# Kernel optimization log

Measured on AMD Instinct MI355X. Metric: run time of the kernel, lower is better.

The kernel has to match this reference:

```python
import jax, jax.numpy as jnp
import numpy as np

D, P, S, E = 200, 200, 150, 150  # drugs, proteins, diseases, side-effects
EMB = 256

def setup_inputs() -> dict:
    key = jax.random.key(0)
    ks = jax.random.split(key, 10)
    s = 0.05
    type_mask = jnp.concatenate([
        jnp.zeros(D, jnp.int64) if False else jnp.full((D,), 0, jnp.int32),
        jnp.full((P,), 1, jnp.int32),
        jnp.full((S,), 2, jnp.int32),
        jnp.full((E,), 3, jnp.int32)]).astype(jnp.int32)
    return {
        'type_mask': type_mask,
        'entity_embedding': jax.random.normal(ks[0], (D + P + S + E, EMB)) * s,
        'relation_embedding': jax.random.normal(ks[1], (1200, EMB)) * s,
        'W_ent': jax.random.normal(ks[2], (EMB, EMB)) * s,
        'W_rel': jax.random.normal(ks[3], (EMB, EMB)) * s,
        'W1': jax.random.normal(ks[4], (2 * EMB, 1024)) * s,
        'b1': jnp.zeros((1024,)),
        'W2': jax.random.normal(ks[5], (1024, 512)) * s,
        'b2': jnp.zeros((512,)),
        'W3': jax.random.normal(ks[6], (512, 2)) * s,
        'b3': jnp.zeros((2,)),
    }

def _pair_softmax(a, b, W1, b1, W2, b2, W3, b3):
    # classifier(concat(a[i], b[j])) for the full cartesian product.
    # First linear is decomposed: W1 @ [a;b] = a@W1a + b@W1b (same math,
    # avoids materializing the [Na*Nb, 2*EMB] concat tensor).
    W1a, W1b = W1[:EMB], W1[EMB:]
    ha = a @ W1a                      # [Na, 1024]
    hb = b @ W1b                      # [Nb, 1024]
    h = jax.nn.relu(ha[:, None, :] + hb[None, :, :] + b1)  # [Na, Nb, 1024]
    h = jax.nn.relu(h @ W2 + b2)      # [Na, Nb, 512]
    logits = h @ W3 + b3              # [Na, Nb, 2]
    Na, Nb = a.shape[0], b.shape[0]
    return jax.nn.softmax(logits.reshape(Na * Nb, 2), axis=-1)

def reference(type_mask, entity_embedding, relation_embedding, W_ent, W_rel,
              W1, b1, W2, b2, W3, b3):
    tm = np.asarray(type_mask)  # concrete, block-structured type ids
    idx = [np.nonzero(tm == t)[0] for t in range(4)]
    # project embeddings (project_on path; nn.Linear: x @ W)
    ent = entity_embedding @ W_ent
    _rel = relation_embedding @ W_rel  # computed in original forward, unused (graph_on off)
    drug, prot, dis, se = (ent[idx[0]], ent[idx[1]], ent[idx[2]], ent[idx[3]])
    cls = lambda a, b: _pair_softmax(a, b, W1, b1, W2, b2, W3, b3)
    out_dp = cls(drug, prot)
    out_dd = cls(drug, drug)
    out_ds = cls(drug, dis)
    out_de = cls(drug, se)
    out_ps = cls(prot, dis)
    out_pp = cls(prot, prot)
    out_pd = cls(prot, drug)
    out_ed = cls(se, drug)
    out_sp = cls(dis, prot)
    out_sd = cls(dis, drug)
    return (out_dp, out_dd, out_ds, out_de, out_ps, out_pp, out_pd,
            out_ed, out_sp, out_sd, drug)
```

## Files before the change

### kernel.cpp

```cpp
#include <hip/hip_runtime.h>
#include <hip/hip_bf16.h>

typedef __attribute__((ext_vector_type(4))) float floatx4;
typedef __attribute__((ext_vector_type(8))) __bf16 bf16x8;
typedef unsigned short ushort_t;

#define NENT  700
#define EMB   256
#define KDIM  1024
#define NDIM  512
#define HROWS 720
#define NPAIR 340000

#define WS_HA   0
#define WS_HB   (WS_HA + HROWS*KDIM*2)
#define WS_W2H  (WS_HB + HROWS*KDIM*2)
#define WS_ENT  (WS_W2H + NDIM*KDIM*2)
#define WS_LG   (WS_ENT + NENT*EMB*4)

__device__ __forceinline__ float ldin(const void* p, int i, int isbf) {
    return isbf ? __bfloat162float(((const __hip_bfloat16*)p)[i])
                : ((const float*)p)[i];
}

__device__ __forceinline__ int detect_bf16(const ushort_t* __restrict__ w) {
    int t = threadIdx.x & 63;
    int e = (w[2*t] >> 7) & 0xFF;
    unsigned long long m = __ballot(e >= 100 && e <= 126);
    return (__popcll(m) >= 48) ? 1 : 0;
}

#define LDS_BARRIER() do { __builtin_amdgcn_s_waitcnt(0xC07F); __builtin_amdgcn_s_barrier(); } while (0)

__global__ void entprep_kernel(const void* __restrict__ E, const void* __restrict__ Went,
                               const void* __restrict__ W2,
                               float* __restrict__ ent, __hip_bfloat16* __restrict__ W2H,
                               void* __restrict__ out) {
    int isbf = detect_bf16((const ushort_t*)E);
    if (blockIdx.x < 88) {
        int ib = blockIdx.x * 8, t = threadIdx.x;
        __shared__ float rows[8][EMB];
#pragma unroll
        for (int r = 0; r < 8; ++r) {
            int i = ib + r;
            rows[r][t] = (i < NENT) ? ldin(E, i*EMB + t, isbf) : 0.f;
        }
        __syncthreads();
        float acc[8] = {0.f,0.f,0.f,0.f,0.f,0.f,0.f,0.f};
        if (isbf) {
            const __hip_bfloat16* W = (const __hip_bfloat16*)Went;
            for (int k = 0; k < EMB; ++k) {
                float w = __bfloat162float(W[k*EMB + t]);
#pragma unroll
                for (int r = 0; r < 8; ++r) acc[r] += rows[r][k] * w;
            }
        } else {
            const float* W = (const float*)Went;
            for (int k = 0; k < EMB; ++k) {
                float w = W[k*EMB + t];
#pragma unroll
                for (int r = 0; r < 8; ++r) acc[r] += rows[r][k] * w;
            }
        }
#pragma unroll
        for (int r = 0; r < 8; ++r) {
            int i = ib + r;
            if (i < NENT) {
                ent[i*EMB + t] = acc[r];
                if (i < 200) {
                    if (isbf) ((__hip_bfloat16*)out)[680000 + i*EMB + t] = __float2bfloat16(acc[r]);
                    else      ((float*)out)[680000 + i*EMB + t] = acc[r];
                }
            }
        }
    } else {
        int g = (blockIdx.x - 88)*256 + threadIdx.x;
        int lane = g & 63, f = (g >> 6) & 15, kc = (g >> 10) & 31, half = g >> 15;
        int l15 = lane & 15, quad = lane >> 4;
        int n = half*256 + f*16 + l15;
        bf16x8 v;
#pragma unroll
        for (int j = 0; j < 8; ++j) {
            int k = kc*32 + quad*8 + j;
            v[j] = (__bf16)ldin(W2, k*NDIM + n, isbf);
        }
        *(bf16x8*)(W2H + (size_t)g*8) = v;
    }
}

__global__ void hab_kernel(const float* __restrict__ ent, const void* __restrict__ E,
                           const void* __restrict__ W1, const void* __restrict__ b1,
                           __hip_bfloat16* __restrict__ HA, __hip_bfloat16* __restrict__ HB) {
    int isbf = detect_bf16((const ushort_t*)E);
    int part = blockIdx.y;
    int ib = blockIdx.x * 16;
    int t = threadIdx.x;
    __shared__ float rows[16][EMB];
#pragma unroll
    for (int r = 0; r < 16; ++r) {
        int i = ib + r;
        rows[r][t] = (i < NENT) ? ent[i*EMB + t] : 0.f;
    }
    __syncthreads();
    float acc[16][4];
#pragma unroll
    for (int r = 0; r < 16; ++r)
#pragma unroll
        for (int p = 0; p < 4; ++p) acc[r][p] = 0.f;

    int wbase = part*EMB*KDIM;
    if (isbf) {
        const __hip_bfloat16* W = (const __hip_bfloat16*)W1;
        for (int k = 0; k < EMB; ++k) {
            float w[4];
#pragma unroll
            for (int p = 0; p < 4; ++p) w[p] = __bfloat162float(W[wbase + k*KDIM + t + p*256]);
#pragma unroll
            for (int r = 0; r < 16; ++r) {
                float e = rows[r][k];
#pragma unroll
                for (int p = 0; p < 4; ++p) acc[r][p] += e * w[p];
            }
        }
    } else {
        const float* W = (const float*)W1;
        for (int k = 0; k < EMB; ++k) {
            float w[4];
#pragma unroll
            for (int p = 0; p < 4; ++p) w[p] = W[wbase + k*KDIM + t + p*256];
#pragma unroll
            for (int r = 0; r < 16; ++r) {
                float e = rows[r][k];
#pragma unroll
                for (int p = 0; p < 4; ++p) acc[r][p] += e * w[p];
            }
        }
    }
    __hip_bfloat16* HX = part ? HB : HA;
#pragma unroll
    for (int r = 0; r < 16; ++r) {
#pragma unroll
        for (int p = 0; p < 4; ++p) {
            int n = t + p*256;
            float v = acc[r][p];
            if (!part) v += ldin(b1, n, isbf);
            HX[(ib + r)*KDIM + n] = __float2bfloat16(v);
        }
    }
}

union U8 { bf16x8 v; unsigned u[4]; };

__device__ __forceinline__ bf16x8 mk_af3(bf16x8 ha, bf16x8 hb) {
    U8 r;
#pragma unroll
    for (int j = 0; j < 4; ++j) {
        float x0 = fmaxf((float)ha[2*j]   + (float)hb[2*j],   0.f);
        float x1 = fmaxf((float)ha[2*j+1] + (float)hb[2*j+1], 0.f);
        unsigned u0 = __float_as_uint(x0) + 0x8000u;
        unsigned u1 = __float_as_uint(x1) + 0x8000u;
#if defined(__has_builtin) && __has_builtin(__builtin_amdgcn_perm)
        r.u[j] = __builtin_amdgcn_perm(u1, u0, 0x07060302u);
#else
        r.u[j] = (u0 >> 16) | (u1 & 0xFFFF0000u);
#endif
    }
    return r.v;
}

#define MFMA(a, b, c) __builtin_amdgcn_mfma_f32_16x16x32_bf16((a), (b), (c), 0, 0, 0)

__global__ __launch_bounds__(512, 2) void pair_kernel(
        const ushort_t* __restrict__ HA, const ushort_t* __restrict__ HB,
        const ushort_t* __restrict__ W2H, const void* __restrict__ E,
        const void* __restrict__ b2, const void* __restrict__ W3,
        const void* __restrict__ b3, void* __restrict__ out) {

    const int blkEnd[10] = {650,1300,1800,2300,2800,3450,4100,4594,5088,5582};
    const int aB[10]  = {0,0,0,0,200,200,200,550,400,400};
    const int bB[10]  = {200,0,400,550,400,200,0,0,200,0};
    const int NaT[10] = {200,200,200,200,200,200,200,150,150,150};
    const int NbT[10] = {200,200,150,150,150,200,200,200,200,200};
    const int jTl[10] = {13,13,10,10,10,13,13,13,13,13};
    const int oOf[10] = {0,80000,160000,220000,280000,340000,420000,500000,560000,620000};

    __shared__ __align__(16) unsigned char sAF[16384];
    __shared__ float lgt[8][64][2];

    int bid = blockIdx.x;
    int ty = 0;
    while (bid >= blkEnd[ty]) ty++;
    int lb = bid - (ty ? blkEnd[ty-1] : 0);
    int jT = jTl[ty];
    int it = lb / jT;
    int jt = lb - it*jT;
    int i0 = aB[ty] + it*4;
    int j0 = bB[ty] + jt*16;

    int tid  = threadIdx.x;
    int lane = tid & 63;
    int w    = tid >> 6;
    int w3_  = w & 3;
    int wh   = w >> 2;
    int l15  = lane & 15;
    int quad = lane >> 4;
    int kb   = (bid*7) & 31;

    const char* WB = (const char*)W2H + ((size_t)(wh*512 + w3_*4))*1024 + lane*16;
    const ushort_t* HBp = HB + (j0 + l15)*KDIM + quad*8;
    const ushort_t* HAp = HA + (i0 + w3_)*KDIM + quad*8;

    floatx4 acc[4][4];
#pragma unroll
    for (int mf = 0; mf < 4; ++mf)
#pragma unroll
        for (int nf = 0; nf < 4; ++nf) acc[mf][nf] = (floatx4){0.f,0.f,0.f,0.f};

    int k0 = kb, k1 = (kb + 1) & 31;
    bf16x8 Bc0 = *(const bf16x8*)(WB + (size_t)k0*16384);
    bf16x8 Bc1 = *(const bf16x8*)(WB + (size_t)k0*16384 + 1024);
    bf16x8 Bc2 = *(const bf16x8*)(WB + (size_t)k0*16384 + 2048);
    bf16x8 Bc3 = *(const bf16x8*)(WB + (size_t)k0*16384 + 3072);
    bf16x8 Bn0 = *(const bf16x8*)(WB + (size_t)k1*16384);
    bf16x8 Bn1 = *(const bf16x8*)(WB + (size_t)k1*16384 + 1024);
    bf16x8 Bn2 = *(const bf16x8*)(WB + (size_t)k1*16384 + 2048);
    bf16x8 Bn3 = *(const bf16x8*)(WB + (size_t)k1*16384 + 3072);

    int kg0 = (kb + wh) & 31;
    bf16x8 ha = *(const bf16x8*)(HAp + kg0*32);
    bf16x8 hb = *(const bf16x8*)(HBp + kg0*32);

#pragma unroll 2
    for (int ph = 0; ph < 16; ++ph) {
        char* sW = (char*)sAF + (ph & 1)*8192 + w*1024 + lane*16;
        *(bf16x8*)sW = mk_af3(ha, hb);
        int kgn = (kb + 2*(ph + 1) + wh) & 31;
        ha = *(const bf16x8*)(HAp + kgn*32);
        hb = *(const bf16x8*)(HBp + kgn*32);
        LDS_BARRIER();

        const char* sR = (const char*)sAF + (ph & 1)*8192 + lane*16;
        int kn2 = (kb + 2*ph + 2) & 31;
        int kn3 = (kb + 2*ph + 3) & 31;
        {
            bf16x8 a0 = *(const bf16x8*)(sR);
            bf16x8 a1 = *(const bf16x8*)(sR + 1024);
            bf16x8 a2 = *(const bf16x8*)(sR + 2048);
            bf16x8 a3 = *(const bf16x8*)(sR + 3072);
            acc[0][0] = MFMA(a0, Bc0, acc[0][0]); acc[1][0] = MFMA(a1, Bc0, acc[1][0]);
            acc[2][0] = MFMA(a2, Bc0, acc[2][0]); acc[3][0] = MFMA(a3, Bc0, acc[3][0]);
            acc[0][1] = MFMA(a0, Bc1, acc[0][1]); acc[1][1] = MFMA(a1, Bc1, acc[1][1]);
            acc[2][1] = MFMA(a2, Bc1, acc[2][1]); acc[3][1] = MFMA(a3, Bc1, acc[3][1]);
            acc[0][2] = MFMA(a0, Bc2, acc[0][2]); acc[1][2] = MFMA(a1, Bc2, acc[1][2]);
            acc[2][2] = MFMA(a2, Bc2, acc[2][2]); acc[3][2] = MFMA(a3, Bc2, acc[3][2]);
            acc[0][3] = MFMA(a0, Bc3, acc[0][3]); acc[1][3] = MFMA(a1, Bc3, acc[1][3]);
            acc[2][3] = MFMA(a2, Bc3, acc[2][3]); acc[3][3] = MFMA(a3, Bc3, acc[3][3]);
        }
        Bc0 = *(const bf16x8*)(WB + (size_t)kn2*16384);
        Bc1 = *(const bf16x8*)(WB + (size_t)kn2*16384 + 1024);
        Bc2 = *(const bf16x8*)(WB + (size_t)kn2*16384 + 2048);
        Bc3 = *(const bf16x8*)(WB + (size_t)kn2*16384 + 3072);
        {
            bf16x8 a0 = *(const bf16x8*)(sR + 4096);
            bf16x8 a1 = *(const bf16x8*)(sR + 4096 + 1024);
            bf16x8 a2 = *(const bf16x8*)(sR + 4096 + 2048);
            bf16x8 a3 = *(const bf16x8*)(sR + 4096 + 3072);
            acc[0][0] = MFMA(a0, Bn0, acc[0][0]); acc[1][0] = MFMA(a1, Bn0, acc[1][0]);
            acc[2][0] = MFMA(a2, Bn0, acc[2][0]); acc[3][0] = MFMA(a3, Bn0, acc[3][0]);
            acc[0][1] = MFMA(a0, Bn1, acc[0][1]); acc[1][1] = MFMA(a1, Bn1, acc[1][1]);
            acc[2][1] = MFMA(a2, Bn1, acc[2][1]); acc[3][1] = MFMA(a3, Bn1, acc[3][1]);
            acc[0][2] = MFMA(a0, Bn2, acc[0][2]); acc[1][2] = MFMA(a1, Bn2, acc[1][2]);
            acc[2][2] = MFMA(a2, Bn2, acc[2][2]); acc[3][2] = MFMA(a3, Bn2, acc[3][2]);
            acc[0][3] = MFMA(a0, Bn3, acc[0][3]); acc[1][3] = MFMA(a1, Bn3, acc[1][3]);
            acc[2][3] = MFMA(a2, Bn3, acc[2][3]); acc[3][3] = MFMA(a3, Bn3, acc[3][3]);
        }
        Bn0 = *(const bf16x8*)(WB + (size_t)kn3*16384);
        Bn1 = *(const bf16x8*)(WB + (size_t)kn3*16384 + 1024);
        Bn2 = *(const bf16x8*)(WB + (size_t)kn3*16384 + 2048);
        Bn3 = *(const bf16x8*)(WB + (size_t)kn3*16384 + 3072);
    }

    int isbf = detect_bf16((const ushort_t*)E);
    int nb = wh*256 + w3_*64;
    float b2v[4], wa[4], wb[4];
#pragma unroll
    for (int nf = 0; nf < 4; ++nf) {
        int n = nb + nf*16 + l15;
        b2v[nf] = ldin(b2, n, isbf);
        wa[nf]  = ldin(W3, 2*n, isbf);
        wb[nf]  = ldin(W3, 2*n+1, isbf);
    }
#pragma unroll
    for (int mf = 0; mf < 4; ++mf) {
        float s0[4] = {0.f,0.f,0.f,0.f};
        float s1[4] = {0.f,0.f,0.f,0.f};
#pragma unroll
        for (int nf = 0; nf < 4; ++nf) {
            floatx4 c = acc[mf][nf];
#pragma unroll
            for (int r = 0; r < 4; ++r) {
                float v = fmaxf(c[r] + b2v[nf], 0.f);
                s0[r] += v * wa[nf];
                s1[r] += v * wb[nf];
            }
        }
#pragma unroll
        for (int off = 1; off < 16; off <<= 1) {
#pragma unroll
            for (int r = 0; r < 4; ++r) {
                s0[r] += __shfl_xor(s0[r], off, 64);
                s1[r] += __shfl_xor(s1[r], off, 64);
            }
        }
        if (l15 == 0) {
#pragma unroll
            for (int r = 0; r < 4; ++r) {
                int p = mf*16 + quad*4 + r;
                lgt[w][p][0] = s0[r];
                lgt[w][p][1] = s1[r];
            }
        }
    }
    __syncthreads();

    if (tid < 64) {
        int p = tid;
        float l0 = 0.f, l1 = 0.f;
#pragma unroll
        for (int ww = 0; ww < 8; ++ww) { l0 += lgt[ww][p][0]; l1 += lgt[ww][p][1]; }
        l0 += ldin(b3, 0, isbf);
        l1 += ldin(b3, 1, isbf);
        int pi = it*4 + (p >> 4), pj = jt*16 + (p & 15);
        if (pi < NaT[ty] && pj < NbT[ty]) {
            float mx = fmaxf(l0, l1);
            float e0 = __expf(l0 - mx), e1 = __expf(l1 - mx);
            float inv = 1.f / (e0 + e1);
            int o = oOf[ty] + (pi*NbT[ty] + pj)*2;
            if (isbf) {
                __hip_bfloat16* ob = (__hip_bfloat16*)out;
                ob[o]   = __float2bfloat16(e0 * inv);
                ob[o+1] = __float2bfloat16(e1 * inv);
            } else {
                float* of = (float*)out;
                of[o]   = e0 * inv;
                of[o+1] = e1 * inv;
            }
        }
    }
}

extern "C" void kernel_launch(void* const* d_in, const int* in_sizes, int n_in,
                              void* d_out, int out_size, void* d_ws, size_t ws_size,
                              hipStream_t stream) {
    const void* E    = d_in[1];
    const void* Went = d_in[3];
    const void* W1   = d_in[5];
    const void* b1   = d_in[6];
    const void* W2   = d_in[7];
    const void* b2   = d_in[8];
    const void* W3   = d_in[9];
    const void* b3   = d_in[10];

    char* ws = (char*)d_ws;
    __hip_bfloat16* HA   = (__hip_bfloat16*)(ws + WS_HA);
    __hip_bfloat16* HB   = (__hip_bfloat16*)(ws + WS_HB);
    __hip_bfloat16* W2H  = (__hip_bfloat16*)(ws + WS_W2H);
    float*          entf = (float*)(ws + WS_ENT);

    entprep_kernel<<<dim3(344), dim3(256), 0, stream>>>(E, Went, W2, entf, W2H, d_out);
    hab_kernel<<<dim3(45, 2), dim3(256), 0, stream>>>(entf, E, W1, b1, HA, HB);
    pair_kernel<<<dim3(5582), dim3(512), 0, stream>>>((const ushort_t*)HA, (const ushort_t*)HB,
                                                      (const ushort_t*)W2H, E, b2, W3, b3, d_out);
}
```

Before: 562.8 us.

## Double pair-kernel M tile to 8 rows so each block reuses W2 fragments twice

```diff
diff --git a/kernel.cpp b/kernel.cpp
--- a/kernel.cpp
+++ b/kernel.cpp
@@ -176,7 +176,7 @@
         const void* __restrict__ b2, const void* __restrict__ W3,
         const void* __restrict__ b3, void* __restrict__ out) {
 
-    const int blkEnd[10] = {650,1300,1800,2300,2800,3450,4100,4594,5088,5582};
+    const int blkEnd[10] = {325,650,900,1150,1400,1725,2050,2297,2544,2791};
     const int aB[10]  = {0,0,0,0,200,200,200,550,400,400};
     const int bB[10]  = {200,0,400,550,400,200,0,0,200,0};
     const int NaT[10] = {200,200,200,200,200,200,200,150,150,150};
@@ -184,8 +184,8 @@
     const int jTl[10] = {13,13,10,10,10,13,13,13,13,13};
     const int oOf[10] = {0,80000,160000,220000,280000,340000,420000,500000,560000,620000};
 
-    __shared__ __align__(16) unsigned char sAF[16384];
-    __shared__ float lgt[8][64][2];
+    __shared__ __align__(16) unsigned char sAF[32768];
+    __shared__ float lgt[8][128][2];
 
     int bid = blockIdx.x;
     int ty = 0;
@@ -194,25 +194,23 @@
     int jT = jTl[ty];
     int it = lb / jT;
     int jt = lb - it*jT;
-    int i0 = aB[ty] + it*4;
+    int i0 = aB[ty] + it*8;
     int j0 = bB[ty] + jt*16;
 
     int tid  = threadIdx.x;
     int lane = tid & 63;
     int w    = tid >> 6;
-    int w3_  = w & 3;
-    int wh   = w >> 2;
     int l15  = lane & 15;
     int quad = lane >> 4;
     int kb   = (bid*7) & 31;
 
-    const char* WB = (const char*)W2H + ((size_t)(wh*512 + w3_*4))*1024 + lane*16;
+    const char* WB = (const char*)W2H + ((size_t)((w>>2)*512 + (w&3)*4))*1024 + lane*16;
     const ushort_t* HBp = HB + (j0 + l15)*KDIM + quad*8;
-    const ushort_t* HAp = HA + (i0 + w3_)*KDIM + quad*8;
-
-    floatx4 acc[4][4];
-#pragma unroll
-    for (int mf = 0; mf < 4; ++mf)
+    const ushort_t* HAp = HA + (i0 + w)*KDIM + quad*8;
+
+    floatx4 acc[8][4];
+#pragma unroll
+    for (int mf = 0; mf < 8; ++mf)
 #pragma unroll
         for (int nf = 0; nf < 4; ++nf) acc[mf][nf] = (floatx4){0.f,0.f,0.f,0.f};
 
@@ -226,53 +224,48 @@
     bf16x8 Bn2 = *(const bf16x8*)(WB + (size_t)k1*16384 + 2048);
     bf16x8 Bn3 = *(const bf16x8*)(WB + (size_t)k1*16384 + 3072);
 
-    int kg0 = (kb + wh) & 31;
-    bf16x8 ha = *(const bf16x8*)(HAp + kg0*32);
-    bf16x8 hb = *(const bf16x8*)(HBp + kg0*32);
+    bf16x8 haA = *(const bf16x8*)(HAp + k0*32);
+    bf16x8 haB = *(const bf16x8*)(HAp + k1*32);
+    bf16x8 hbA = *(const bf16x8*)(HBp + k0*32);
+    bf16x8 hbB = *(const bf16x8*)(HBp + k1*32);
 
 #pragma unroll 2
     for (int ph = 0; ph < 16; ++ph) {
-        char* sW = (char*)sAF + (ph & 1)*8192 + w*1024 + lane*16;
-        *(bf16x8*)sW = mk_af3(ha, hb);
-        int kgn = (kb + 2*(ph + 1) + wh) & 31;
-        ha = *(const bf16x8*)(HAp + kgn*32);
-        hb = *(const bf16x8*)(HBp + kgn*32);
-        LDS_BARRIER();
-
-        const char* sR = (const char*)sAF + (ph & 1)*8192 + lane*16;
+        char* sW = (char*)sAF + (ph & 1)*16384 + w*1024 + lane*16;
+        *(bf16x8*)(sW)        = mk_af3(haA, hbA);
+        *(bf16x8*)(sW + 8192) = mk_af3(haB, hbB);
         int kn2 = (kb + 2*ph + 2) & 31;
         int kn3 = (kb + 2*ph + 3) & 31;
+        haA = *(const bf16x8*)(HAp + kn2*32);
+        haB = *(const bf16x8*)(HAp + kn3*32);
+        hbA = *(const bf16x8*)(HBp + kn2*32);
+        hbB = *(const bf16x8*)(HBp + kn3*32);
+        LDS_BARRIER();
+
+        const char* sR = (const char*)sAF + (ph & 1)*16384 + lane*16;
         {
-            bf16x8 a0 = *(const bf16x8*)(sR);
-            bf16x8 a1 = *(const bf16x8*)(sR + 1024);
-            bf16x8 a2 = *(const bf16x8*)(sR + 2048);
-            bf16x8 a3 = *(const bf16x8*)(sR + 3072);
-            acc[0][0] = MFMA(a0, Bc0, acc[0][0]); acc[1][0] = MFMA(a1, Bc0, acc[1][0]);
-            acc[2][0] = MFMA(a2, Bc0, acc[2][0]); acc[3][0] = MFMA(a3, Bc0, acc[3][0]);
-            acc[0][1] = MFMA(a0, Bc1, acc[0][1]); acc[1][1] = MFMA(a1, Bc1, acc[1][1]);
-            acc[2][1] = MFMA(a2, Bc1, acc[2][1]); acc[3][1] = MFMA(a3, Bc1, acc[3][1]);
-            acc[0][2] = MFMA(a0, Bc2, acc[0][2]); acc[1][2] = MFMA(a1, Bc2, acc[1][2]);
-            acc[2][2] = MFMA(a2, Bc2, acc[2][2]); acc[3][2] = MFMA(a3, Bc2, acc[3][2]);
-            acc[0][3] = MFMA(a0, Bc3, acc[0][3]); acc[1][3] = MFMA(a1, Bc3, acc[1][3]);
-            acc[2][3] = MFMA(a2, Bc3, acc[2][3]); acc[3][3] = MFMA(a3, Bc3, acc[3][3]);
+#pragma unroll
+            for (int mf = 0; mf < 8; ++mf) {
+                bf16x8 a = *(const bf16x8*)(sR + mf*1024);
+                acc[mf][0] = MFMA(a, Bc0, acc[mf][0]);
+                acc[mf][1] = MFMA(a, Bc1, acc[mf][1]);
+                acc[mf][2] = MFMA(a, Bc2, acc[mf][2]);
+                acc[mf][3] = MFMA(a, Bc3, acc[mf][3]);
+            }
         }
         Bc0 = *(const bf16x8*)(WB + (size_t)kn2*16384);
         Bc1 = *(const bf16x8*)(WB + (size_t)kn2*16384 + 1024);
         Bc2 = *(const bf16x8*)(WB + (size_t)kn2*16384 + 2048);
         Bc3 = *(const bf16x8*)(WB + (size_t)kn2*16384 + 3072);
         {
-            bf16x8 a0 = *(const bf16x8*)(sR + 4096);
-            bf16x8 a1 = *(const bf16x8*)(sR + 4096 + 1024);
-            bf16x8 a2 = *(const bf16x8*)(sR + 4096 + 2048);
-            bf16x8 a3 = *(const bf16x8*)(sR + 4096 + 3072);
-            acc[0][0] = MFMA(a0, Bn0, acc[0][0]); acc[1][0] = MFMA(a1, Bn0, acc[1][0]);
-            acc[2][0] = MFMA(a2, Bn0, acc[2][0]); acc[3][0] = MFMA(a3, Bn0, acc[3][0]);
-            acc[0][1] = MFMA(a0, Bn1, acc[0][1]); acc[1][1] = MFMA(a1, Bn1, acc[1][1]);
-            acc[2][1] = MFMA(a2, Bn1, acc[2][1]); acc[3][1] = MFMA(a3, Bn1, acc[3][1]);
-            acc[0][2] = MFMA(a0, Bn2, acc[0][2]); acc[1][2] = MFMA(a1, Bn2, acc[1][2]);
-            acc[2][2] = MFMA(a2, Bn2, acc[2][2]); acc[3][2] = MFMA(a3, Bn2, acc[3][2]);
-            acc[0][3] = MFMA(a0, Bn3, acc[0][3]); acc[1][3] = MFMA(a1, Bn3, acc[1][3]);
-            acc[2][3] = MFMA(a2, Bn3, acc[2][3]); acc[3][3] = MFMA(a3, Bn3, acc[3][3]);
+#pragma unroll
+            for (int mf = 0; mf < 8; ++mf) {
+                bf16x8 a = *(const bf16x8*)(sR + 8192 + mf*1024);
+                acc[mf][0] = MFMA(a, Bn0, acc[mf][0]);
+                acc[mf][1] = MFMA(a, Bn1, acc[mf][1]);
+                acc[mf][2] = MFMA(a, Bn2, acc[mf][2]);
+                acc[mf][3] = MFMA(a, Bn3, acc[mf][3]);
+            }
         }
         Bn0 = *(const bf16x8*)(WB + (size_t)kn3*16384);
         Bn1 = *(const bf16x8*)(WB + (size_t)kn3*16384 + 1024);
@@ -281,7 +274,7 @@
     }
 
     int isbf = detect_bf16((const ushort_t*)E);
-    int nb = wh*256 + w3_*64;
+    int nb = w*64;
     float b2v[4], wa[4], wb[4];
 #pragma unroll
     for (int nf = 0; nf < 4; ++nf) {
@@ -291,7 +284,7 @@
         wb[nf]  = ldin(W3, 2*n+1, isbf);
     }
 #pragma unroll
-    for (int mf = 0; mf < 4; ++mf) {
+    for (int mf = 0; mf < 8; ++mf) {
         float s0[4] = {0.f,0.f,0.f,0.f};
         float s1[4] = {0.f,0.f,0.f,0.f};
 #pragma unroll
@@ -323,14 +316,14 @@
     }
     __syncthreads();
 
-    if (tid < 64) {
+    if (tid < 128) {
         int p = tid;
         float l0 = 0.f, l1 = 0.f;
 #pragma unroll
         for (int ww = 0; ww < 8; ++ww) { l0 += lgt[ww][p][0]; l1 += lgt[ww][p][1]; }
         l0 += ldin(b3, 0, isbf);
         l1 += ldin(b3, 1, isbf);
-        int pi = it*4 + (p >> 4), pj = jt*16 + (p & 15);
+        int pi = it*8 + (p >> 4), pj = jt*16 + (p & 15);
         if (pi < NaT[ty] && pj < NbT[ty]) {
             float mx = fmaxf(l0, l1);
             float e0 = __expf(l0 - mx), e1 = __expf(l1 - mx);
@@ -369,6 +362,6 @@
 
     entprep_kernel<<<dim3(344), dim3(256), 0, stream>>>(E, Went, W2, entf, W2H, d_out);
     hab_kernel<<<dim3(45, 2), dim3(256), 0, stream>>>(entf, E, W1, b1, HA, HB);
-    pair_kernel<<<dim3(5582), dim3(512), 0, stream>>>((const ushort_t*)HA, (const ushort_t*)HB,
+    pair_kernel<<<dim3(2791), dim3(512), 0, stream>>>((const ushort_t*)HA, (const ushort_t*)HB,
                                                       (const ushort_t*)W2H, E, b2, W3, b3, d_out);
 }
```

After: 507.1 us. -9.9%, faster.
